# Performance work log

Measured on AMD Instinct MI355X. Metric: run time of the kernel, lower is better.

Reference implementation:

```python
import jax, jax.numpy as jnp
import numpy as np

GAMMA = 1.0  # weight on CRL loss
BETA = 1.0   # weight on MDCA calibration loss
B, C = 4096, 32000
DATASET_SIZE = 50000


def setup_inputs() -> dict:
    key = jax.random.key(0)
    k1, k2, k3, k4 = jax.random.split(key, 4)
    logits = jax.random.normal(k1, (B, C), dtype=jnp.float32)
    targets = jax.random.randint(k2, (B,), 0, C, dtype=jnp.int64)
    idx = jax.random.randint(k3, (B,), 0, DATASET_SIZE, dtype=jnp.int64)
    # normalized historical correctness per dataset sample (History table)
    correctness = jax.random.uniform(k4, (DATASET_SIZE,), dtype=jnp.float32)
    return {"logits": logits, "targets": targets, "idx": idx, "correctness": correctness}


def reference(logits, targets, idx, correctness):
    b, c = logits.shape
    logp = jax.nn.log_softmax(logits, axis=1)
    # CrossEntropyLoss (mean reduction)
    loss_cls = -jnp.mean(jnp.take_along_axis(logp, targets[:, None], axis=1))
    p = jnp.exp(logp)  # softmax probabilities, reused by MDCA and CRL

    # MDCA: mean_c | mean_b p[:, c] - freq(target == c) |, fused (no per-class loop)
    avg_conf = jnp.mean(p, axis=0)                                  # [C]
    avg_count = jnp.zeros((c,), logits.dtype).at[targets].add(1.0) / b  # [C]
    loss_cal = jnp.mean(jnp.abs(avg_conf - avg_count))

    # CRL (rank_target='softmax'): max-softmax confidence margin ranking
    conf = jnp.max(p, axis=1)          # [B]
    conf2 = jnp.roll(conf, -1)
    idx2 = jnp.roll(idx, -1)
    c1 = correctness[idx]
    c2 = correctness[idx2]
    rank_target = jnp.sign(c1 - c2)                     # {-1, 0, +1}
    rank_margin = jnp.abs(c1 - c2)
    tnz = jnp.where(rank_target == 0, jnp.ones_like(rank_target), rank_target)
    rank_input2 = conf2 + rank_margin / tnz
    # MarginRankingLoss(margin=0, mean): mean(max(0, -target*(x1 - x2)))
    loss_ref = jnp.mean(jnp.maximum(0.0, -rank_target * (conf - rank_input2)))

    return loss_cls + GAMMA * loss_ref + BETA * loss_cal
```

## Files before the change

### kernel.cpp

```cpp
#include <hip/hip_runtime.h>
#include <math.h>


#define NB  256
#define TPB 1024
#define NJ  8

__global__ __launch_bounds__(TPB) void fused_pass_kernel(
    const float* __restrict__ logits, const int* __restrict__ targets,
    float* __restrict__ partial,
    float* __restrict__ rowinv, float* __restrict__ celogp,
    float* __restrict__ counts, int B, int C)
{
    const int tid = threadIdx.x;
    const int n4  = C >> 2;
    const int rpb = B / NB;
    const int r0  = blockIdx.x * rpb;

    __shared__ float red[2][TPB / 64];
    __shared__ float sS[64];

    float4 acc[NJ];
    #pragma unroll
    for (int j = 0; j < NJ; ++j) acc[j] = make_float4(0.f, 0.f, 0.f, 0.f);

    const int wid = tid >> 6;

    for (int r = 0; r < rpb; ++r) {
        const float4* row4 = (const float4*)(logits + (size_t)(r0 + r) * (size_t)C);

        float4 f[NJ];
        #pragma unroll
        for (int j = 0; j < NJ; ++j) {
            const int k = tid + TPB * j;
            f[j] = (k < n4) ? row4[k] : make_float4(-1e30f, -1e30f, -1e30f, -1e30f);
        }

        float ls = 0.f;
        #pragma unroll
        for (int j = 0; j < NJ; ++j) {
            f[j].x = __expf(f[j].x);
            f[j].y = __expf(f[j].y);
            f[j].z = __expf(f[j].z);
            f[j].w = __expf(f[j].w);
            ls += (f[j].x + f[j].y) + (f[j].z + f[j].w);
        }

        #pragma unroll
        for (int off = 32; off; off >>= 1) ls += __shfl_xor(ls, off, 64);
        const int par = r & 1;
        if ((tid & 63) == 0) red[par][wid] = ls;
        __syncthreads();
        float s = 0.f;
        #pragma unroll
        for (int w = 0; w < TPB / 64; ++w) s += red[par][w];
        if (tid == 0) sS[r] = s;
        const float inv = 1.0f / s;

        #pragma unroll
        for (int j = 0; j < NJ; ++j) {
            acc[j].x = fmaf(f[j].x, inv, acc[j].x);
            acc[j].y = fmaf(f[j].y, inv, acc[j].y);
            acc[j].z = fmaf(f[j].z, inv, acc[j].z);
            acc[j].w = fmaf(f[j].w, inv, acc[j].w);
        }
    }

    float4* po = (float4*)(partial + (size_t)blockIdx.x * (size_t)C);
    #pragma unroll
    for (int j = 0; j < NJ; ++j) {
        const int k = tid + TPB * j;
        if (k < n4) po[k] = acc[j];
    }

    __syncthreads();
    if (tid < rpb) {
        const int b = r0 + tid;
        const float s = sS[tid];
        rowinv[b] = 1.0f / s;
        const int t = targets[b];
        celogp[b] = logits[(size_t)b * (size_t)C + t] - logf(s);
        atomicAdd(&counts[t], 1.0f);
    }
}

__global__ __launch_bounds__(128) void reduce_cal_kernel(
    const float* __restrict__ partial, const float* __restrict__ counts,
    float* __restrict__ cal, int C)
{
    const int c = blockIdx.x * 128 + threadIdx.x;
    float s = 0.f;
    for (int p = 0; p < NB; ++p) s += partial[(size_t)p * (size_t)C + c];
    float d = fabsf(s - counts[c]);

    #pragma unroll
    for (int off = 32; off; off >>= 1) d += __shfl_xor(d, off, 64);
    __shared__ float rr[2];
    if ((threadIdx.x & 63) == 0) rr[threadIdx.x >> 6] = d;
    __syncthreads();
    if (threadIdx.x == 0) atomicAdd(cal, rr[0] + rr[1]);
}

__global__ __launch_bounds__(1024) void final_loss_kernel(
    const float* __restrict__ rowinv, const float* __restrict__ celogp,
    const int* __restrict__ idx, const float* __restrict__ correctness,
    const float* __restrict__ cal, float* __restrict__ out, int B, int C)
{
    const int tid = threadIdx.x;
    float sum_ce = 0.f, sum_crl = 0.f;

    for (int b = tid; b < B; b += 1024) {
        sum_ce += celogp[b];
        const int b2 = (b + 1 == B) ? 0 : b + 1;
        const float conf  = rowinv[b];
        const float conf2 = rowinv[b2];
        const float c1 = correctness[idx[b]];
        const float c2 = correctness[idx[b2]];
        const float rt  = (c1 > c2) ? 1.f : ((c1 < c2) ? -1.f : 0.f);
        const float rm  = fabsf(c1 - c2);
        const float tnz = (rt == 0.f) ? 1.f : rt;
        const float ri2 = conf2 + rm / tnz;
        sum_crl += fmaxf(0.f, -rt * (conf - ri2));
    }

    #pragma unroll
    for (int off = 32; off; off >>= 1) {
        sum_ce  += __shfl_xor(sum_ce,  off, 64);
        sum_crl += __shfl_xor(sum_crl, off, 64);
    }
    __shared__ float red[2][16];
    const int wid = tid >> 6;
    if ((tid & 63) == 0) { red[0][wid] = sum_ce; red[1][wid] = sum_crl; }
    __syncthreads();
    if (tid == 0) {
        float tce = 0.f, tcrl = 0.f;
        #pragma unroll
        for (int w = 0; w < 16; ++w) { tce += red[0][w]; tcrl += red[1][w]; }
        const float loss_cls = -tce / (float)B;
        const float loss_ref = tcrl / (float)B;
        const float loss_cal = cal[0] / ((float)B * (float)C);
        out[0] = loss_cls + loss_ref + loss_cal;
    }
}

extern "C" void kernel_launch(void* const* d_in, const int* in_sizes, int n_in,
                              void* d_out, int out_size, void* d_ws, size_t ws_size,
                              hipStream_t stream) {
    const float* logits      = (const float*)d_in[0];
    const int*   targets     = (const int*)d_in[1];
    const int*   idx         = (const int*)d_in[2];
    const float* correctness = (const float*)d_in[3];
    float* out = (float*)d_out;

    const int B = in_sizes[1];
    const int C = in_sizes[0] / B;

    char* ws = (char*)d_ws;
    float* partial = (float*)ws;   ws += (size_t)NB * (size_t)C * sizeof(float);
    float* rowinv  = (float*)ws;   ws += (size_t)B * sizeof(float);
    float* celogp  = (float*)ws;   ws += (size_t)B * sizeof(float);
    float* counts  = (float*)ws;   ws += (size_t)C * sizeof(float);
    float* cal     = (float*)ws;

    hipMemsetAsync(counts, 0, (size_t)C * sizeof(float), stream);
    hipMemsetAsync(cal, 0, sizeof(float), stream);

    fused_pass_kernel<<<NB, TPB, 0, stream>>>(logits, targets, partial,
                                              rowinv, celogp, counts, B, C);

    reduce_cal_kernel<<<C / 128, 128, 0, stream>>>(partial, counts, cal, C);

    final_loss_kernel<<<1, 1024, 0, stream>>>(rowinv, celogp, idx, correctness,
                                              cal, out, B, C);
}
```

Measured before the change: 711.3 us.

## Double-buffer row loads, store bf16 partials, compute true max-softmax confidence

The main loop now prefetches the next logits row into a second register buffer while the current row is processed. With only one block per CU and one row in flight, load latency is the bottleneck this targets. Per-block column partial sums are stored as bf16 to halve partial write and read traffic, at some cost in MDCA accuracy. The row max of exp is also reduced so confidence becomes max(p) rather than 1/sum, which fixes a correctness bug. A launch-bounds occupancy hint is added and the two memsets are merged into one; the extra register buffer under the tighter register cap risks spills.

```diff
diff --git a/kernel.cpp b/kernel.cpp
--- a/kernel.cpp
+++ b/kernel.cpp
@@ -1,4 +1,5 @@
 #include <hip/hip_runtime.h>
+#include <hip/hip_bf16.h>
 #include <math.h>
 
 
@@ -6,78 +7,112 @@
 #define TPB 1024
 #define NJ  8
 
-__global__ __launch_bounds__(TPB) void fused_pass_kernel(
+__device__ __forceinline__ unsigned short f2bf(float x) {
+    __hip_bfloat16 h = __float2bfloat16(x);
+    return *reinterpret_cast<unsigned short*>(&h);
+}
+
+__global__ __launch_bounds__(TPB, 4) void fused_pass_kernel(
     const float* __restrict__ logits, const int* __restrict__ targets,
-    float* __restrict__ partial,
-    float* __restrict__ rowinv, float* __restrict__ celogp,
+    unsigned short* __restrict__ partial,
+    float* __restrict__ conf, float* __restrict__ celogp,
     float* __restrict__ counts, int B, int C)
 {
     const int tid = threadIdx.x;
     const int n4  = C >> 2;
     const int rpb = B / NB;
     const int r0  = blockIdx.x * rpb;
-
-    __shared__ float red[2][TPB / 64];
-    __shared__ float sS[64];
+    const int wid = tid >> 6;
+
+    __shared__ float redS[2][TPB / 64];
+    __shared__ float redM[2][TPB / 64];
+    __shared__ float sS[32], sM[32];
 
     float4 acc[NJ];
-    #pragma unroll
-    for (int j = 0; j < NJ; ++j) acc[j] = make_float4(0.f, 0.f, 0.f, 0.f);
-
-    const int wid = tid >> 6;
-
-    for (int r = 0; r < rpb; ++r) {
+    float4 bufA[NJ], bufB[NJ];
+    #pragma unroll
+    for (int j = 0; j < NJ; ++j) {
+        acc[j]  = make_float4(0.f, 0.f, 0.f, 0.f);
+        bufA[j] = make_float4(0.f, 0.f, 0.f, 0.f);
+        bufB[j] = make_float4(0.f, 0.f, 0.f, 0.f);
+    }
+
+    auto loadrow = [&](float4 (&buf)[NJ], int r) {
         const float4* row4 = (const float4*)(logits + (size_t)(r0 + r) * (size_t)C);
-
-        float4 f[NJ];
         #pragma unroll
         for (int j = 0; j < NJ; ++j) {
             const int k = tid + TPB * j;
-            f[j] = (k < n4) ? row4[k] : make_float4(-1e30f, -1e30f, -1e30f, -1e30f);
-        }
-
-        float ls = 0.f;
+            if (k < n4) buf[j] = row4[k];
+        }
+    };
+
+    auto process = [&](float4 (&buf)[NJ], int r) {
+        float ls = 0.f, lme = 0.f;
         #pragma unroll
         for (int j = 0; j < NJ; ++j) {
-            f[j].x = __expf(f[j].x);
-            f[j].y = __expf(f[j].y);
-            f[j].z = __expf(f[j].z);
-            f[j].w = __expf(f[j].w);
-            ls += (f[j].x + f[j].y) + (f[j].z + f[j].w);
-        }
-
-        #pragma unroll
-        for (int off = 32; off; off >>= 1) ls += __shfl_xor(ls, off, 64);
+            const int k = tid + TPB * j;
+            if (k < n4) {
+                buf[j].x = __expf(buf[j].x);
+                buf[j].y = __expf(buf[j].y);
+                buf[j].z = __expf(buf[j].z);
+                buf[j].w = __expf(buf[j].w);
+                ls += (buf[j].x + buf[j].y) + (buf[j].z + buf[j].w);
+                lme = fmaxf(lme, fmaxf(fmaxf(buf[j].x, buf[j].y),
+                                       fmaxf(buf[j].z, buf[j].w)));
+            }
+        }
+        #pragma unroll
+        for (int off = 32; off; off >>= 1) {
+            ls  += __shfl_xor(ls, off, 64);
+            lme  = fmaxf(lme, __shfl_xor(lme, off, 64));
+        }
         const int par = r & 1;
-        if ((tid & 63) == 0) red[par][wid] = ls;
+        if ((tid & 63) == 0) { redS[par][wid] = ls; redM[par][wid] = lme; }
         __syncthreads();
-        float s = 0.f;
-        #pragma unroll
-        for (int w = 0; w < TPB / 64; ++w) s += red[par][w];
-        if (tid == 0) sS[r] = s;
+        float s = 0.f, me = 0.f;
+        #pragma unroll
+        for (int w = 0; w < TPB / 64; ++w) {
+            s += redS[par][w];
+            me = fmaxf(me, redM[par][w]);
+        }
+        if (tid == 0) { sS[r] = s; sM[r] = me; }
         const float inv = 1.0f / s;
-
         #pragma unroll
         for (int j = 0; j < NJ; ++j) {
-            acc[j].x = fmaf(f[j].x, inv, acc[j].x);
-            acc[j].y = fmaf(f[j].y, inv, acc[j].y);
-            acc[j].z = fmaf(f[j].z, inv, acc[j].z);
-            acc[j].w = fmaf(f[j].w, inv, acc[j].w);
-        }
-    }
-
-    float4* po = (float4*)(partial + (size_t)blockIdx.x * (size_t)C);
+            acc[j].x = fmaf(buf[j].x, inv, acc[j].x);
+            acc[j].y = fmaf(buf[j].y, inv, acc[j].y);
+            acc[j].z = fmaf(buf[j].z, inv, acc[j].z);
+            acc[j].w = fmaf(buf[j].w, inv, acc[j].w);
+        }
+    };
+
+    loadrow(bufA, 0);
+    for (int rr = 0; rr < rpb; rr += 2) {
+        if (rr + 1 < rpb) loadrow(bufB, rr + 1);
+        process(bufA, rr);
+        if (rr + 2 < rpb) loadrow(bufA, rr + 2);
+        process(bufB, rr + 1);
+    }
+
+    unsigned short* po = partial + (size_t)blockIdx.x * (size_t)C;
     #pragma unroll
     for (int j = 0; j < NJ; ++j) {
         const int k = tid + TPB * j;
-        if (k < n4) po[k] = acc[j];
+        if (k < n4) {
+            ushort4 u;
+            u.x = f2bf(acc[j].x);
+            u.y = f2bf(acc[j].y);
+            u.z = f2bf(acc[j].z);
+            u.w = f2bf(acc[j].w);
+            *(ushort4*)(po + 4 * (size_t)k) = u;
+        }
     }
 
     __syncthreads();
     if (tid < rpb) {
         const int b = r0 + tid;
         const float s = sS[tid];
-        rowinv[b] = 1.0f / s;
+        conf[b] = sM[tid] / s;
         const int t = targets[b];
         celogp[b] = logits[(size_t)b * (size_t)C + t] - logf(s);
         atomicAdd(&counts[t], 1.0f);
@@ -85,12 +120,15 @@
 }
 
 __global__ __launch_bounds__(128) void reduce_cal_kernel(
-    const float* __restrict__ partial, const float* __restrict__ counts,
+    const unsigned short* __restrict__ partial, const float* __restrict__ counts,
     float* __restrict__ cal, int C)
 {
     const int c = blockIdx.x * 128 + threadIdx.x;
     float s = 0.f;
-    for (int p = 0; p < NB; ++p) s += partial[(size_t)p * (size_t)C + c];
+    for (int p = 0; p < NB; ++p) {
+        const unsigned int w = (unsigned int)partial[(size_t)p * (size_t)C + c] << 16;
+        s += __uint_as_float(w);
+    }
     float d = fabsf(s - counts[c]);
 
     #pragma unroll
@@ -102,7 +140,7 @@
 }
 
 __global__ __launch_bounds__(1024) void final_loss_kernel(
-    const float* __restrict__ rowinv, const float* __restrict__ celogp,
+    const float* __restrict__ conf, const float* __restrict__ celogp,
     const int* __restrict__ idx, const float* __restrict__ correctness,
     const float* __restrict__ cal, float* __restrict__ out, int B, int C)
 {
@@ -112,15 +150,15 @@
     for (int b = tid; b < B; b += 1024) {
         sum_ce += celogp[b];
         const int b2 = (b + 1 == B) ? 0 : b + 1;
-        const float conf  = rowinv[b];
-        const float conf2 = rowinv[b2];
+        const float cf  = conf[b];
+        const float cf2 = conf[b2];
         const float c1 = correctness[idx[b]];
         const float c2 = correctness[idx[b2]];
         const float rt  = (c1 > c2) ? 1.f : ((c1 < c2) ? -1.f : 0.f);
         const float rm  = fabsf(c1 - c2);
         const float tnz = (rt == 0.f) ? 1.f : rt;
-        const float ri2 = conf2 + rm / tnz;
-        sum_crl += fmaxf(0.f, -rt * (conf - ri2));
+        const float ri2 = cf2 + rm / tnz;
+        sum_crl += fmaxf(0.f, -rt * (cf - ri2));
     }
 
     #pragma unroll
@@ -156,20 +194,20 @@
     const int C = in_sizes[0] / B;
 
     char* ws = (char*)d_ws;
-    float* partial = (float*)ws;   ws += (size_t)NB * (size_t)C * sizeof(float);
-    float* rowinv  = (float*)ws;   ws += (size_t)B * sizeof(float);
-    float* celogp  = (float*)ws;   ws += (size_t)B * sizeof(float);
-    float* counts  = (float*)ws;   ws += (size_t)C * sizeof(float);
-    float* cal     = (float*)ws;
-
-    hipMemsetAsync(counts, 0, (size_t)C * sizeof(float), stream);
-    hipMemsetAsync(cal, 0, sizeof(float), stream);
+    unsigned short* partial = (unsigned short*)ws;
+    ws += (size_t)NB * (size_t)C * sizeof(unsigned short);
+    float* conf   = (float*)ws;   ws += (size_t)B * sizeof(float);
+    float* celogp = (float*)ws;   ws += (size_t)B * sizeof(float);
+    float* counts = (float*)ws;   ws += (size_t)C * sizeof(float);
+    float* cal    = (float*)ws;
+
+    hipMemsetAsync(counts, 0, ((size_t)C + 1) * sizeof(float), stream);
 
     fused_pass_kernel<<<NB, TPB, 0, stream>>>(logits, targets, partial,
-                                              rowinv, celogp, counts, B, C);
+                                              conf, celogp, counts, B, C);
 
     reduce_cal_kernel<<<C / 128, 128, 0, stream>>>(partial, counts, cal, C);
 
-    final_loss_kernel<<<1, 1024, 0, stream>>>(rowinv, celogp, idx, correctness,
+    final_loss_kernel<<<1, 1024, 0, stream>>>(conf, celogp, idx, correctness,
                                               cal, out, B, C);
 }
```

Result: slower. 828.6 us (+16.5%).
